# Performance work log

Measured on AMD Instinct MI355X. Metric: run time of the kernel, lower is better.

The kernel has to match this reference:

```python
import jax, jax.numpy as jnp
import numpy as np

NUM_ENT = 100000   # entity vocabulary
NUM_EDGES = 200000 # KB pairs processed per hop (max_act)
D = 768            # BERT hidden size
NSTEP = 3          # num hops
QLEN = 32          # question length


def setup_inputs() -> dict:
    key = jax.random.key(0)
    ks = jax.random.split(key, 18)
    rn = lambda k, s, scale=1.0: jax.random.normal(k, s, dtype=jnp.float32) * scale
    W = 0.02  # weight init scale
    return {
        "q_emb": rn(ks[0], (1, D)),
        "q_word_h": rn(ks[1], (1, QLEN, D)),
        "desc_emb": rn(ks[2], (NUM_EDGES, D)),
        "step_w1": rn(ks[3], (NSTEP, D, D), W),
        "step_b1": rn(ks[4], (NSTEP, D), W),
        "step_w2": rn(ks[5], (NSTEP, D, D), W),
        "step_b2": rn(ks[6], (NSTEP, D), W),
        "rel_w1": rn(ks[7], (D, 256), W),
        "rel_b1": rn(ks[8], (256,), W),
        "rel_w2": rn(ks[9], (256,), W),
        "rel_b2": rn(ks[10], (1,), W),
        "hop_w1": rn(ks[11], (D, 256), W),
        "hop_b1": rn(ks[12], (256,), W),
        "hop_w2": rn(ks[13], (256, NSTEP), W),
        "hop_b2": rn(ks[14], (NSTEP,), W),
        "kb_pair": jax.random.randint(ks[15], (NUM_EDGES, 2), 0, NUM_ENT, dtype=jnp.int32),
        "topic_ent_idxs": jax.random.randint(ks[16], (4,), 0, NUM_ENT, dtype=jnp.int32),
    }


def reference(q_emb, q_word_h, desc_emb, step_w1, step_b1, step_w2, step_b2,
              rel_w1, rel_b1, rel_w2, rel_b2, hop_w1, hop_b1, hop_w2, hop_b2,
              kb_pair, topic_ent_idxs):
    gelu = lambda x: jax.nn.gelu(x, approximate=False)  # torch nn.GELU default
    # topic entity one-hot init (idx_to_one_hot)
    last_e = jnp.zeros((NUM_ENT,), jnp.float32).at[topic_ent_idxs].set(1.0)
    sub, obj = kb_pair[:, 0], kb_pair[:, 1]
    ent_probs = []
    for t in range(NSTEP):
        # step encoder: Linear -> GELU -> Linear
        cq = gelu(q_emb @ step_w1[t] + step_b1[t]) @ step_w2[t] + step_b2[t]  # [1,D]
        # attention over question words
        q_logits = jnp.einsum('bd,bld->bl', cq, q_word_h)                      # [1,L]
        q_dist = jax.nn.softmax(q_logits, axis=1)
        ctx = jnp.einsum('bl,bld->bd', q_dist, q_word_h) + cq                  # [1,D]
        # relation classifier over edge descriptions: Linear -> GELU -> Linear
        h = gelu((ctx * desc_emb) @ rel_w1 + rel_b1)                           # [E,256]
        d_prob = jax.nn.sigmoid(h @ rel_w2 + rel_b2)                           # [E]
        # follow: gather subject scores, scatter-add to objects
        obj_p = last_e[sub] * d_prob
        last_e = jax.ops.segment_sum(obj_p, obj, num_segments=NUM_ENT)
        # clamp-style renormalization (detached divisor)
        z = jax.lax.stop_gradient(jnp.where(last_e > 1.0, last_e, 1.0))
        last_e = last_e / z
        ent_probs.append(last_e)
    hop_res = jnp.stack(ent_probs, 0)                                          # [T,N]
    hop_attn = jax.nn.softmax(gelu(q_emb @ hop_w1 + hop_b1) @ hop_w2 + hop_b2, axis=1)  # [1,T]
    return (hop_attn @ hop_res)[0]                                             # [N]
```

## Files before the change

kernel.cpp:

```cpp
#include <hip/hip_runtime.h>
#include <math.h>

#define NUM_ENT 100000
#define NUM_EDGES 200000
#define DIM 768
#define BM 64
#define KSTEPS 24
#define NC 16
#define DCH 48

typedef float f32x4 __attribute__((ext_vector_type(4)));
typedef __bf16 bf16x8 __attribute__((ext_vector_type(8)));

#define WS_Y1    0
#define WS_CQ    2304
#define WS_HA    4704
#define WS_HOP1  4736
#define WS_CTX   4992
#define WS_B     7424
#define WS_DPROB 302336
#define WS_P1    302336
#define WS_P1H   339200
#define WS_P2    343296
#define WS_E     902336

__device__ __forceinline__ unsigned short f2bf(float f) {
    unsigned int x = __builtin_bit_cast(unsigned int, f);
    x = x + 0x7fffu + ((x >> 16) & 1u);
    return (unsigned short)(x >> 16);
}

__device__ __forceinline__ float gelu_f(float x) {
    float z = 0.70710678118654752f * x;
    float s = fabsf(z);
    float t = 1.f / (1.f + 0.3275911f * s);
    float p = t * (0.254829592f + t * (-0.284496736f + t * (1.421413741f +
              t * (-1.453152027f + t * 1.061405429f))));
    float e = __expf(-s * s);
    float erfa = copysignf(1.f - p * e, z);
    return 0.5f * x * (1.f + erfa);
}

__global__ void k1a(const float* __restrict__ q, const float* __restrict__ sw1,
                    const float* __restrict__ hw1, float* __restrict__ ws) {
    int b = blockIdx.x, tid = threadIdx.x;
    if (b < 48) {
        int t = b >> 4, c = b & 15;
        const float* w = sw1 + (size_t)t * DIM * DIM + (size_t)c * DCH * DIM;
        float a0 = 0.f, a1 = 0.f, a2 = 0.f;
        for (int d = 0; d < DCH; ++d) {
            float qv = q[c * DCH + d];
            const float* wr = w + (size_t)d * DIM;
            a0 += qv * wr[tid]; a1 += qv * wr[tid + 256]; a2 += qv * wr[tid + 512];
        }
        float* p = ws + WS_P1 + (size_t)b * DIM;
        p[tid] = a0; p[tid + 256] = a1; p[tid + 512] = a2;
    } else {
        int c = b - 48;
        const float* w = hw1 + (size_t)c * DCH * 256;
        float a0 = 0.f;
        for (int d = 0; d < DCH; ++d) a0 += q[c * DCH + d] * w[(size_t)d * 256 + tid];
        ws[WS_P1H + c * 256 + tid] = a0;
    }
}

__global__ void k1b(const float* __restrict__ sb1, const float* __restrict__ hb1,
                    float* __restrict__ ws) {
    int o = blockIdx.x * 256 + threadIdx.x;
    if (o < 2304) {
        int t = o / DIM, j = o % DIM;
        float s = sb1[o];
        for (int c = 0; c < NC; ++c) s += ws[WS_P1 + (size_t)(t * 16 + c) * DIM + j];
        ws[WS_Y1 + o] = gelu_f(s);
    } else if (o < 2560) {
        int j = o - 2304;
        float s = hb1[j];
        for (int c = 0; c < NC; ++c) s += ws[WS_P1H + c * 256 + j];
        ws[WS_HOP1 + j] = gelu_f(s);
    }
}

__global__ void k2a(const float* __restrict__ sw2, float* __restrict__ ws) {
    int b = blockIdx.x, tid = threadIdx.x;
    int t = b >> 4, c = b & 15;
    const float* w = sw2 + (size_t)t * DIM * DIM + (size_t)c * DCH * DIM;
    const float* y = ws + WS_Y1 + t * DIM + c * DCH;
    float a0 = 0.f, a1 = 0.f, a2 = 0.f;
    for (int d = 0; d < DCH; ++d) {
        float yv = y[d];
        const float* wr = w + (size_t)d * DIM;
        a0 += yv * wr[tid]; a1 += yv * wr[tid + 256]; a2 += yv * wr[tid + 512];
    }
    float* p = ws + WS_P2 + (size_t)b * DIM;
    p[tid] = a0; p[tid + 256] = a1; p[tid + 512] = a2;
}

__global__ void k2b(const float* __restrict__ sb2, float* __restrict__ ws) {
    int o = blockIdx.x * 256 + threadIdx.x;
    int t = o / DIM, j = o % DIM;
    float s = sb2[o];
    for (int c = 0; c < NC; ++c) s += ws[WS_P2 + (size_t)(t * 16 + c) * DIM + j];
    ws[WS_CQ + o] = s;
}

__global__ void k345(const float* __restrict__ qwh, const float* __restrict__ hw2,
                     const float* __restrict__ hb2, float* __restrict__ ws) {
    __shared__ float qlog[96];
    int tid = threadIdx.x;
    int w = tid >> 6, lane = tid & 63;
    for (int s = 0; s < 6; ++s) {
        int p = w * 6 + s;
        int t = p >> 5, l = p & 31;
        const float* c = ws + WS_CQ + t * DIM;
        const float* qw = qwh + l * DIM;
        float acc = 0.f;
        for (int i = lane; i < DIM; i += 64) acc += c[i] * qw[i];
        for (int m = 32; m; m >>= 1) acc += __shfl_xor(acc, m);
        if (lane == 0) qlog[p] = acc;
    }
    __syncthreads();
    if (tid < 64) {
        for (int t = 0; t < 3; ++t) {
            float v = (lane < 32) ? qlog[t * 32 + lane] : -1e30f;
            float mx = v;
            for (int m = 1; m < 32; m <<= 1) mx = fmaxf(mx, __shfl_xor(mx, m, 32));
            float e = (lane < 32) ? __expf(v - mx) : 0.f;
            float s = e;
            for (int m = 1; m < 32; m <<= 1) s += __shfl_xor(s, m, 32);
            if (lane < 32) qlog[t * 32 + lane] = e / s;
        }
        float lg = 0.f;
        if (lane < 3) {
            for (int s = 0; s < 256; ++s) lg += ws[WS_HOP1 + s] * hw2[s * 3 + lane];
            lg += hb2[lane];
        }
        float l0 = __shfl(lg, 0), l1 = __shfl(lg, 1), l2 = __shfl(lg, 2);
        if (lane == 0) {
            float mx = fmaxf(l0, fmaxf(l1, l2));
            float e0 = __expf(l0 - mx), e1 = __expf(l1 - mx), e2 = __expf(l2 - mx);
            float s = e0 + e1 + e2;
            ws[WS_HA + 0] = e0 / s; ws[WS_HA + 1] = e1 / s; ws[WS_HA + 2] = e2 / s;
        }
    }
    __syncthreads();
    for (int o = tid; o < 2304; o += 1024) {
        int t = o / DIM, d = o % DIM;
        float acc = ws[WS_CQ + o];
        const float* qd = qlog + t * 32;
        for (int l = 0; l < 32; ++l) acc += qd[l] * qwh[l * DIM + d];
        ws[WS_CTX + o] = acc;
    }
}

__global__ void k6_bmat(const float* __restrict__ rw1, float* __restrict__ ws) {
    int g = blockIdx.x * 256 + threadIdx.x;
    int lane = g & 63, f = g >> 6;
    int ks = f / 48, r = f % 48;
    int t = r >> 4, cf = r & 15;
    int k0 = ks * 32 + (lane >> 4) * 8;
    int col = cf * 16 + (lane & 15);
    const float* ctx = ws + WS_CTX + t * DIM;
    union { unsigned short u[8]; bf16x8 v; } pk;
    #pragma unroll
    for (int j = 0; j < 8; ++j) {
        float v = ctx[k0 + j] * rw1[(size_t)(k0 + j) * 256 + col];
        pk.u[j] = f2bf(v);
    }
    *(bf16x8*)((unsigned short*)(ws + WS_B) + (size_t)g * 8) = pk.v;
}

#define MFMA4(A, B0, B1, B2, B3, RF)                                               \
    acc[RF][0] = __builtin_amdgcn_mfma_f32_16x16x32_bf16(A, B0, acc[RF][0], 0,0,0); \
    acc[RF][1] = __builtin_amdgcn_mfma_f32_16x16x32_bf16(A, B1, acc[RF][1], 0,0,0); \
    acc[RF][2] = __builtin_amdgcn_mfma_f32_16x16x32_bf16(A, B2, acc[RF][2], 0,0,0); \
    acc[RF][3] = __builtin_amdgcn_mfma_f32_16x16x32_bf16(A, B3, acc[RF][3], 0,0,0);

__global__ __launch_bounds__(768, 3)
void k7_gemm(const float* __restrict__ desc, const float* __restrict__ rb1,
             const float* __restrict__ rw2, const float* __restrict__ rb2,
             float* __restrict__ ws) {
    extern __shared__ char lds[];
    unsigned short* aLds = (unsigned short*)lds;
    float* part = (float*)(lds + 98304);

    const unsigned short* bmat = (const unsigned short*)(ws + WS_B);
    float* dprob = ws + WS_DPROB;
    int tid = threadIdx.x, blk = blockIdx.x;
    int wid = tid >> 6, lane = tid & 63;
    int t = wid >> 2, cg = wid & 3;
    int fbase = (t << 4) + (cg << 2);

    const unsigned short* bp = bmat + ((size_t)fbase << 9) + lane * 8;
    bf16x8 b0_0 = *(const bf16x8*)(bp);
    bf16x8 b0_1 = *(const bf16x8*)(bp + 512);
    bf16x8 b0_2 = *(const bf16x8*)(bp + 1024);
    bf16x8 b0_3 = *(const bf16x8*)(bp + 1536);
    bp += 48 * 512;

    #pragma unroll
    for (int i = 0; i < 8; ++i) {
        int gf = i * 768 + tid;
        int l = gf & 63, f = gf >> 6;
        int ks = f >> 2, rf = f & 3;
        int row = rf * 16 + (l & 15);
        int kb = ks * 32 + (l >> 4) * 8;
        const float* src = desc + (size_t)(blk * BM + row) * DIM + kb;
        float4 v0 = *(const float4*)src;
        float4 v1 = *(const float4*)(src + 4);
        bf16x8 pk;
        pk[0] = (__bf16)v0.x; pk[1] = (__bf16)v0.y; pk[2] = (__bf16)v0.z; pk[3] = (__bf16)v0.w;
        pk[4] = (__bf16)v1.x; pk[5] = (__bf16)v1.y; pk[6] = (__bf16)v1.z; pk[7] = (__bf16)v1.w;
        *(bf16x8*)(aLds + (size_t)f * 512 + l * 8) = pk;
    }
    __syncthreads();

    f32x4 acc[4][4];
    #pragma unroll
    for (int rf = 0; rf < 4; ++rf)
        #pragma unroll
        for (int i = 0; i < 4; ++i) acc[rf][i] = f32x4{0.f, 0.f, 0.f, 0.f};

    const unsigned short* ab0 = aLds + lane * 8;
    bf16x8 b1_0, b1_1, b1_2, b1_3;

    #pragma unroll 1
    for (int ks = 0; ks < KSTEPS; ks += 2) {
        b1_0 = *(const bf16x8*)(bp);
        b1_1 = *(const bf16x8*)(bp + 512);
        b1_2 = *(const bf16x8*)(bp + 1024);
        b1_3 = *(const bf16x8*)(bp + 1536);
        bp += 48 * 512;
        {
            const unsigned short* ab = ab0 + (size_t)ks * 2048;
            bf16x8 a;
            a = *(const bf16x8*)(ab);          MFMA4(a, b0_0, b0_1, b0_2, b0_3, 0)
            a = *(const bf16x8*)(ab + 512);    MFMA4(a, b0_0, b0_1, b0_2, b0_3, 1)
            a = *(const bf16x8*)(ab + 1024);   MFMA4(a, b0_0, b0_1, b0_2, b0_3, 2)
            a = *(const bf16x8*)(ab + 1536);   MFMA4(a, b0_0, b0_1, b0_2, b0_3, 3)
        }
        if (ks + 2 < KSTEPS) {
            b0_0 = *(const bf16x8*)(bp);
            b0_1 = *(const bf16x8*)(bp + 512);
            b0_2 = *(const bf16x8*)(bp + 1024);
            b0_3 = *(const bf16x8*)(bp + 1536);
            bp += 48 * 512;
        }
        {
            const unsigned short* ab = ab0 + (size_t)ks * 2048 + 2048;
            bf16x8 a;
            a = *(const bf16x8*)(ab);          MFMA4(a, b1_0, b1_1, b1_2, b1_3, 0)
            a = *(const bf16x8*)(ab + 512);    MFMA4(a, b1_0, b1_1, b1_2, b1_3, 1)
            a = *(const bf16x8*)(ab + 1024);   MFMA4(a, b1_0, b1_1, b1_2, b1_3, 2)
            a = *(const bf16x8*)(ab + 1536);   MFMA4(a, b1_0, b1_1, b1_2, b1_3, 3)
        }
    }

    int col16 = lane & 15, quart = lane >> 4;
    float b1v[4], w2v[4];
    #pragma unroll
    for (int i = 0; i < 4; ++i) {
        int c = cg * 64 + i * 16 + col16;
        b1v[i] = rb1[c]; w2v[i] = rw2[c];
    }
    #pragma unroll
    for (int rf = 0; rf < 4; ++rf) {
        #pragma unroll
        for (int r = 0; r < 4; ++r) {
            float s = 0.f;
            #pragma unroll
            for (int i = 0; i < 4; ++i)
                s += gelu_f(acc[rf][i][r] + b1v[i]) * w2v[i];
            #pragma unroll
            for (int m = 1; m < 16; m <<= 1) s += __shfl_xor(s, m);
            if (col16 == 0) part[wid * 64 + rf * 16 + quart * 4 + r] = s;
        }
    }
    __syncthreads();
    if (tid < 192) {
        int tt = tid >> 6, row = tid & 63;
        float v = part[(tt * 4 + 0) * 64 + row] + part[(tt * 4 + 1) * 64 + row]
                + part[(tt * 4 + 2) * 64 + row] + part[(tt * 4 + 3) * 64 + row] + rb2[0];
        float p = 1.f / (1.f + __expf(-v));
        dprob[(size_t)tt * NUM_EDGES + blk * BM + row] = p;
    }
}

__global__ void kzero(float* __restrict__ ws) {
    int i = blockIdx.x * 256 + threadIdx.x;
    if (i < 3 * NUM_ENT) ws[WS_E + NUM_ENT + i] = 0.f;
}

__global__ void k9_scatter(const int* __restrict__ kb, const int* __restrict__ topics,
                           float* __restrict__ ws, int t) {
    int e = blockIdx.x * 256 + threadIdx.x;
    if (e >= NUM_EDGES) return;
    int sub = kb[2 * e], obj = kb[2 * e + 1];
    float g;
    if (t == 0) {
        g = (sub == topics[0] || sub == topics[1] || sub == topics[2] || sub == topics[3]) ? 1.f : 0.f;
    } else {
        float v = ws[WS_E + (size_t)t * NUM_ENT + sub];
        g = v / fmaxf(v, 1.f);
    }
    float p = g * ws[WS_DPROB + (size_t)t * NUM_EDGES + e];
    if (p != 0.f) atomicAdd(&ws[WS_E + (size_t)(t + 1) * NUM_ENT + obj], p);
}

__global__ void kout(const float* __restrict__ ws, float* __restrict__ out) {
    int i = blockIdx.x * 256 + threadIdx.x;
    if (i >= NUM_ENT) return;
    float v1 = ws[WS_E + 1 * NUM_ENT + i]; v1 /= fmaxf(v1, 1.f);
    float v2 = ws[WS_E + 2 * NUM_ENT + i]; v2 /= fmaxf(v2, 1.f);
    float v3 = ws[WS_E + 3 * NUM_ENT + i]; v3 /= fmaxf(v3, 1.f);
    out[i] = ws[WS_HA + 0] * v1 + ws[WS_HA + 1] * v2 + ws[WS_HA + 2] * v3;
}

extern "C" void kernel_launch(void* const* d_in, const int* in_sizes, int n_in,
                              void* d_out, int out_size, void* d_ws, size_t ws_size,
                              hipStream_t stream) {
    const float* q_emb   = (const float*)d_in[0];
    const float* qwh     = (const float*)d_in[1];
    const float* desc    = (const float*)d_in[2];
    const float* sw1     = (const float*)d_in[3];
    const float* sb1     = (const float*)d_in[4];
    const float* sw2     = (const float*)d_in[5];
    const float* sb2     = (const float*)d_in[6];
    const float* rw1     = (const float*)d_in[7];
    const float* rb1     = (const float*)d_in[8];
    const float* rw2     = (const float*)d_in[9];
    const float* rb2     = (const float*)d_in[10];
    const float* hw1     = (const float*)d_in[11];
    const float* hb1     = (const float*)d_in[12];
    const float* hw2     = (const float*)d_in[13];
    const float* hb2     = (const float*)d_in[14];
    const int*   kb      = (const int*)d_in[15];
    const int*   topics  = (const int*)d_in[16];
    float* ws  = (float*)d_ws;
    float* out = (float*)d_out;

    int nblk7 = NUM_EDGES / BM;

    kzero<<<(3 * NUM_ENT + 255) / 256, 256, 0, stream>>>(ws);
    k1a<<<64, 256, 0, stream>>>(q_emb, sw1, hw1, ws);
    k1b<<<10, 256, 0, stream>>>(sb1, hb1, ws);
    k2a<<<48, 256, 0, stream>>>(sw2, ws);
    k2b<<<9, 256, 0, stream>>>(sb2, ws);
    k345<<<1, 1024, 0, stream>>>(qwh, hw2, hb2, ws);
    k6_bmat<<<288, 256, 0, stream>>>(rw1, ws);
    k7_gemm<<<nblk7, 768, 101376, stream>>>(desc, rb1, rw2, rb2, ws);
    for (int t = 0; t < 3; ++t)
        k9_scatter<<<(NUM_EDGES + 255) / 256, 256, 0, stream>>>(kb, topics, ws, t);
    kout<<<(NUM_ENT + 255) / 256, 256, 0, stream>>>(ws, out);
}
```

Measured before the change: 463.5 us.

## Apply ctx scaling to A tile in LDS instead of three pre-scaled B matrices

The per-hop ctx vector is no longer folded into three separate bf16 copies of rel_w1. The GEMM kernel now keeps a single shared B, loads ctx into LDS, and scales each bf16 desc fragment by ctx for each of the three hops before issuing MFMAs. Warps are reorganized (512 threads, 2 row halves x 4 column groups) so each warp accumulates all three hops for 32 rows. This cuts B global traffic and the B prep kernel to a third, at the cost of extra VALU unpack/multiply/convert work in the inner loop and more accumulator registers.

```diff
diff --git a/kernel.cpp b/kernel.cpp
--- a/kernel.cpp
+++ b/kernel.cpp
@@ -155,51 +155,86 @@
 __global__ void k6_bmat(const float* __restrict__ rw1, float* __restrict__ ws) {
     int g = blockIdx.x * 256 + threadIdx.x;
     int lane = g & 63, f = g >> 6;
-    int ks = f / 48, r = f % 48;
-    int t = r >> 4, cf = r & 15;
+    int ks = f >> 4, cf = f & 15;
     int k0 = ks * 32 + (lane >> 4) * 8;
     int col = cf * 16 + (lane & 15);
-    const float* ctx = ws + WS_CTX + t * DIM;
     union { unsigned short u[8]; bf16x8 v; } pk;
     #pragma unroll
-    for (int j = 0; j < 8; ++j) {
-        float v = ctx[k0 + j] * rw1[(size_t)(k0 + j) * 256 + col];
-        pk.u[j] = f2bf(v);
-    }
+    for (int j = 0; j < 8; ++j)
+        pk.u[j] = f2bf(rw1[(size_t)(k0 + j) * 256 + col]);
     *(bf16x8*)((unsigned short*)(ws + WS_B) + (size_t)g * 8) = pk.v;
 }
 
-#define MFMA4(A, B0, B1, B2, B3, RF)                                               \
-    acc[RF][0] = __builtin_amdgcn_mfma_f32_16x16x32_bf16(A, B0, acc[RF][0], 0,0,0); \
-    acc[RF][1] = __builtin_amdgcn_mfma_f32_16x16x32_bf16(A, B1, acc[RF][1], 0,0,0); \
-    acc[RF][2] = __builtin_amdgcn_mfma_f32_16x16x32_bf16(A, B2, acc[RF][2], 0,0,0); \
-    acc[RF][3] = __builtin_amdgcn_mfma_f32_16x16x32_bf16(A, B3, acc[RF][3], 0,0,0);
-
-__global__ __launch_bounds__(768, 3)
+#define KSTEP(KS, B0, B1, B2, B3)                                                   \
+  {                                                                                  \
+    const unsigned short* ab = aLds + ((size_t)((KS) * 4 + rh * 2)) * 512 + lane * 8;\
+    bf16x8 a0r = *(const bf16x8*)ab;                                                 \
+    bf16x8 a1r = *(const bf16x8*)(ab + 512);                                         \
+    const float* cp = ctxL + (KS) * 32 + khi;                                        \
+    float a0f[8], a1f[8];                                                            \
+    _Pragma("unroll")                                                                \
+    for (int p = 0; p < 4; ++p) {                                                    \
+      unsigned int r0 = ((const unsigned int*)&a0r)[p];                              \
+      unsigned int r1 = ((const unsigned int*)&a1r)[p];                              \
+      a0f[2*p]   = __builtin_bit_cast(float, r0 << 16);                              \
+      a0f[2*p+1] = __builtin_bit_cast(float, r0 & 0xffff0000u);                      \
+      a1f[2*p]   = __builtin_bit_cast(float, r1 << 16);                              \
+      a1f[2*p+1] = __builtin_bit_cast(float, r1 & 0xffff0000u);                      \
+    }                                                                                \
+    _Pragma("unroll")                                                                \
+    for (int t = 0; t < 3; ++t) {                                                    \
+      float4 cA = *(const float4*)(cp + t * DIM);                                    \
+      float4 cB2 = *(const float4*)(cp + t * DIM + 4);                               \
+      float cc[8] = {cA.x, cA.y, cA.z, cA.w, cB2.x, cB2.y, cB2.z, cB2.w};            \
+      bf16x8 s0, s1;                                                                 \
+      _Pragma("unroll")                                                              \
+      for (int p = 0; p < 4; ++p) {                                                  \
+        unsigned int w0, w1;                                                         \
+        asm("v_cvt_pk_bf16_f32 %0, %1, %2" : "=v"(w0)                                \
+            : "v"(a0f[2*p] * cc[2*p]), "v"(a0f[2*p+1] * cc[2*p+1]));                 \
+        asm("v_cvt_pk_bf16_f32 %0, %1, %2" : "=v"(w1)                                \
+            : "v"(a1f[2*p] * cc[2*p]), "v"(a1f[2*p+1] * cc[2*p+1]));                 \
+        ((unsigned int*)&s0)[p] = w0;                                                \
+        ((unsigned int*)&s1)[p] = w1;                                                \
+      }                                                                              \
+      acc[t][0][0] = __builtin_amdgcn_mfma_f32_16x16x32_bf16(s0, B0, acc[t][0][0], 0,0,0); \
+      acc[t][0][1] = __builtin_amdgcn_mfma_f32_16x16x32_bf16(s0, B1, acc[t][0][1], 0,0,0); \
+      acc[t][0][2] = __builtin_amdgcn_mfma_f32_16x16x32_bf16(s0, B2, acc[t][0][2], 0,0,0); \
+      acc[t][0][3] = __builtin_amdgcn_mfma_f32_16x16x32_bf16(s0, B3, acc[t][0][3], 0,0,0); \
+      acc[t][1][0] = __builtin_amdgcn_mfma_f32_16x16x32_bf16(s1, B0, acc[t][1][0], 0,0,0); \
+      acc[t][1][1] = __builtin_amdgcn_mfma_f32_16x16x32_bf16(s1, B1, acc[t][1][1], 0,0,0); \
+      acc[t][1][2] = __builtin_amdgcn_mfma_f32_16x16x32_bf16(s1, B2, acc[t][1][2], 0,0,0); \
+      acc[t][1][3] = __builtin_amdgcn_mfma_f32_16x16x32_bf16(s1, B3, acc[t][1][3], 0,0,0); \
+    }                                                                                \
+  }
+
+__global__ __launch_bounds__(512, 2)
 void k7_gemm(const float* __restrict__ desc, const float* __restrict__ rb1,
              const float* __restrict__ rw2, const float* __restrict__ rb2,
              float* __restrict__ ws) {
     extern __shared__ char lds[];
     unsigned short* aLds = (unsigned short*)lds;
-    float* part = (float*)(lds + 98304);
+    float* ctxL = (float*)(lds + 98304);
+    float* part = (float*)(lds + 107520);
 
     const unsigned short* bmat = (const unsigned short*)(ws + WS_B);
+    const float* ctxg = ws + WS_CTX;
     float* dprob = ws + WS_DPROB;
     int tid = threadIdx.x, blk = blockIdx.x;
     int wid = tid >> 6, lane = tid & 63;
-    int t = wid >> 2, cg = wid & 3;
-    int fbase = (t << 4) + (cg << 2);
-
-    const unsigned short* bp = bmat + ((size_t)fbase << 9) + lane * 8;
+    int rh = wid >> 2, cg = wid & 3;
+    int khi = (lane >> 4) * 8;
+
+    const unsigned short* bp = bmat + ((size_t)(cg * 4) << 9) + lane * 8;
     bf16x8 b0_0 = *(const bf16x8*)(bp);
     bf16x8 b0_1 = *(const bf16x8*)(bp + 512);
     bf16x8 b0_2 = *(const bf16x8*)(bp + 1024);
     bf16x8 b0_3 = *(const bf16x8*)(bp + 1536);
-    bp += 48 * 512;
-
-    #pragma unroll
-    for (int i = 0; i < 8; ++i) {
-        int gf = i * 768 + tid;
+    bp += 16 * 512;
+
+    #pragma unroll
+    for (int i = 0; i < 12; ++i) {
+        int gf = i * 512 + tid;
         int l = gf & 63, f = gf >> 6;
         int ks = f >> 2, rf = f & 3;
         int row = rf * 16 + (l & 15);
@@ -212,15 +247,17 @@
         pk[4] = (__bf16)v1.x; pk[5] = (__bf16)v1.y; pk[6] = (__bf16)v1.z; pk[7] = (__bf16)v1.w;
         *(bf16x8*)(aLds + (size_t)f * 512 + l * 8) = pk;
     }
+    for (int o = tid; o < 2304; o += 512) ctxL[o] = ctxg[o];
     __syncthreads();
 
-    f32x4 acc[4][4];
-    #pragma unroll
-    for (int rf = 0; rf < 4; ++rf)
+    f32x4 acc[3][2][4];
+    #pragma unroll
+    for (int t = 0; t < 3; ++t)
         #pragma unroll
-        for (int i = 0; i < 4; ++i) acc[rf][i] = f32x4{0.f, 0.f, 0.f, 0.f};
-
-    const unsigned short* ab0 = aLds + lane * 8;
+        for (int rf = 0; rf < 2; ++rf)
+            #pragma unroll
+            for (int i = 0; i < 4; ++i) acc[t][rf][i] = f32x4{0.f, 0.f, 0.f, 0.f};
+
     bf16x8 b1_0, b1_1, b1_2, b1_3;
 
     #pragma unroll 1
@@ -229,30 +266,16 @@
         b1_1 = *(const bf16x8*)(bp + 512);
         b1_2 = *(const bf16x8*)(bp + 1024);
         b1_3 = *(const bf16x8*)(bp + 1536);
-        bp += 48 * 512;
-        {
-            const unsigned short* ab = ab0 + (size_t)ks * 2048;
-            bf16x8 a;
-            a = *(const bf16x8*)(ab);          MFMA4(a, b0_0, b0_1, b0_2, b0_3, 0)
-            a = *(const bf16x8*)(ab + 512);    MFMA4(a, b0_0, b0_1, b0_2, b0_3, 1)
-            a = *(const bf16x8*)(ab + 1024);   MFMA4(a, b0_0, b0_1, b0_2, b0_3, 2)
-            a = *(const bf16x8*)(ab + 1536);   MFMA4(a, b0_0, b0_1, b0_2, b0_3, 3)
-        }
+        bp += 16 * 512;
+        KSTEP(ks, b0_0, b0_1, b0_2, b0_3)
         if (ks + 2 < KSTEPS) {
             b0_0 = *(const bf16x8*)(bp);
             b0_1 = *(const bf16x8*)(bp + 512);
             b0_2 = *(const bf16x8*)(bp + 1024);
             b0_3 = *(const bf16x8*)(bp + 1536);
-            bp += 48 * 512;
-        }
-        {
-            const unsigned short* ab = ab0 + (size_t)ks * 2048 + 2048;
-            bf16x8 a;
-            a = *(const bf16x8*)(ab);          MFMA4(a, b1_0, b1_1, b1_2, b1_3, 0)
-            a = *(const bf16x8*)(ab + 512);    MFMA4(a, b1_0, b1_1, b1_2, b1_3, 1)
-            a = *(const bf16x8*)(ab + 1024);   MFMA4(a, b1_0, b1_1, b1_2, b1_3, 2)
-            a = *(const bf16x8*)(ab + 1536);   MFMA4(a, b1_0, b1_1, b1_2, b1_3, 3)
-        }
+            bp += 16 * 512;
+        }
+        KSTEP(ks + 1, b1_0, b1_1, b1_2, b1_3)
     }
 
     int col16 = lane & 15, quart = lane >> 4;
@@ -263,23 +286,25 @@
         b1v[i] = rb1[c]; w2v[i] = rw2[c];
     }
     #pragma unroll
-    for (int rf = 0; rf < 4; ++rf) {
+    for (int t = 0; t < 3; ++t)
         #pragma unroll
-        for (int r = 0; r < 4; ++r) {
-            float s = 0.f;
+        for (int rf = 0; rf < 2; ++rf)
             #pragma unroll
-            for (int i = 0; i < 4; ++i)
-                s += gelu_f(acc[rf][i][r] + b1v[i]) * w2v[i];
-            #pragma unroll
-            for (int m = 1; m < 16; m <<= 1) s += __shfl_xor(s, m);
-            if (col16 == 0) part[wid * 64 + rf * 16 + quart * 4 + r] = s;
-        }
-    }
+            for (int r = 0; r < 4; ++r) {
+                float s = 0.f;
+                #pragma unroll
+                for (int i = 0; i < 4; ++i)
+                    s += gelu_f(acc[t][rf][i][r] + b1v[i]) * w2v[i];
+                #pragma unroll
+                for (int m = 1; m < 16; m <<= 1) s += __shfl_xor(s, m);
+                if (col16 == 0)
+                    part[(cg * 3 + t) * 64 + rh * 32 + rf * 16 + quart * 4 + r] = s;
+            }
     __syncthreads();
     if (tid < 192) {
         int tt = tid >> 6, row = tid & 63;
-        float v = part[(tt * 4 + 0) * 64 + row] + part[(tt * 4 + 1) * 64 + row]
-                + part[(tt * 4 + 2) * 64 + row] + part[(tt * 4 + 3) * 64 + row] + rb2[0];
+        float v = part[(0 * 3 + tt) * 64 + row] + part[(1 * 3 + tt) * 64 + row]
+                + part[(2 * 3 + tt) * 64 + row] + part[(3 * 3 + tt) * 64 + row] + rb2[0];
         float p = 1.f / (1.f + __expf(-v));
         dprob[(size_t)tt * NUM_EDGES + blk * BM + row] = p;
     }
@@ -346,8 +371,8 @@
     k2a<<<48, 256, 0, stream>>>(sw2, ws);
     k2b<<<9, 256, 0, stream>>>(sb2, ws);
     k345<<<1, 1024, 0, stream>>>(qwh, hw2, hb2, ws);
-    k6_bmat<<<288, 256, 0, stream>>>(rw1, ws);
-    k7_gemm<<<nblk7, 768, 101376, stream>>>(desc, rb1, rw2, rb2, ws);
+    k6_bmat<<<96, 256, 0, stream>>>(rw1, ws);
+    k7_gemm<<<nblk7, 512, 110592, stream>>>(desc, rb1, rw2, rb2, ws);
     for (int t = 0; t < 3; ++t)
         k9_scatter<<<(NUM_EDGES + 255) / 256, 256, 0, stream>>>(kb, topics, ws, t);
     kout<<<(NUM_ENT + 255) / 256, 256, 0, stream>>>(ws, out);
```

Measured after the change: 552.7 us. 19.3% more time.
